# Kernel optimization log

Hardware: AMD Instinct MI355X
Metric: run time of the kernel (lower is better)

## Reference

```python
import jax, jax.numpy as jnp
import numpy as np

N, E, D, H, F = 50000, 800000, 256, 4, 32
NEG_SLOPE = 0.2

def setup_inputs() -> dict:
    key = jax.random.key(0)
    ks = jax.random.split(key, 8)
    h = jax.random.normal(ks[0], (N, D), dtype=jnp.float32)
    W = jax.random.normal(ks[1], (D, H * F), dtype=jnp.float32) * (1.0 / np.sqrt(D))
    attn_l_w = jax.random.normal(ks[2], (F, 1), dtype=jnp.float32) * (1.0 / np.sqrt(F))
    attn_l_b = jnp.zeros((1,), dtype=jnp.float32)
    attn_r_w = jax.random.normal(ks[3], (F, 1), dtype=jnp.float32) * (1.0 / np.sqrt(F))
    attn_r_b = jnp.zeros((1,), dtype=jnp.float32)
    bias = jnp.zeros((H, F), dtype=jnp.float32)
    src = jax.random.randint(ks[4], (E,), 0, N, dtype=jnp.int32)
    dst = jax.random.randint(ks[5], (E,), 0, N, dtype=jnp.int32)
    return {"h": h, "W": W, "attn_l_w": attn_l_w, "attn_l_b": attn_l_b,
            "attn_r_w": attn_r_w, "attn_r_b": attn_r_b, "bias": bias,
            "src": src, "dst": dst}

def reference(h, W, attn_l_w, attn_l_b, attn_r_w, attn_r_b, bias, src, dst):
    # node projection: [N, D] @ [D, H*F] -> [N, H, F]
    hW = (h @ W).reshape(N, H, F)
    # per-node attention halves: Dense(1) over F -> [N, H, 1]
    el = jnp.einsum('nhf,fo->nho', hW, attn_l_w) + attn_l_b
    er = jnp.einsum('nhf,fo->nho', hW, attn_r_w) + attn_r_b
    # edge logits: src contributes er, dst contributes el -> [E, H, 1]
    e = er[src] + el[dst]
    e = jnp.where(e >= 0, e, NEG_SLOPE * e)  # leaky_relu
    # segment softmax over destination groups
    emax = jax.ops.segment_max(e, dst, num_segments=N)  # [N, H, 1]
    ee = jnp.exp(e - emax[dst])
    denom = jax.ops.segment_sum(ee, dst, num_segments=N)  # [N, H, 1]
    a = ee / denom[dst]  # [E, H, 1]
    # weighted message scatter-sum: [E, H, F] -> [N, H, F]
    m = hW[src] * a
    out = jax.ops.segment_sum(m, dst, num_segments=N) + bias
    return out
```

## Files before the change

kernel.cpp:

```cpp
#include <hip/hip_runtime.h>
#include <hip/hip_bf16.h>

#define N_NODES 50000
#define E_EDGES 800000
#define D_IN    256
#define H_HEADS 4
#define HF      128
#define NEG_SLOPE 0.2f
#define SCAN_BLOCKS ((N_NODES + 255) / 256)
#define PREP_BLOCKS 128
#define ZERO_BLOCKS SCAN_BLOCKS
#define GEMM_BLOCKS ((N_NODES + 63) / 64)

#define HIST_FAT_BLOCKS 625
#define HIST_STRIDE (HIST_FAT_BLOCKS * 256)

#define FILL_BLOCKS 782
#define FILL_STRIDE (FILL_BLOCKS * 256)

typedef __attribute__((ext_vector_type(8))) short bf16x8;
typedef __attribute__((ext_vector_type(4))) float f32x4;

__device__ __forceinline__ float bf_lo(unsigned u) { return __uint_as_float(u << 16); }
__device__ __forceinline__ float bf_hi(unsigned u) { return __uint_as_float(u & 0xFFFF0000u); }

__global__ __launch_bounds__(256) void k_zero_prep(unsigned* __restrict__ cnt,
                                                   const float* __restrict__ W,
                                                   __hip_bfloat16* __restrict__ Wt) {
    const int b = blockIdx.x;
    if (b < ZERO_BLOCKS) {
        const int g = b * 256 + threadIdx.x;
        if (g < N_NODES) cnt[g] = 0u;
    } else {
        const int g = (b - ZERO_BLOCKS) * 256 + threadIdx.x;
        const int n = g >> 8;
        const int k = g & 255;
        Wt[n * D_IN + k] = __float2bfloat16(W[k * HF + n]);
    }
}

__global__ __launch_bounds__(256) void k_gemm_hist(const float* __restrict__ h,
                                                   const __hip_bfloat16* __restrict__ Wt,
                                                   const float* __restrict__ lw,
                                                   const float* __restrict__ lb,
                                                   const float* __restrict__ rw,
                                                   const float* __restrict__ rb,
                                                   __hip_bfloat16* __restrict__ hW,
                                                   float* __restrict__ el,
                                                   float* __restrict__ er,
                                                   const int* __restrict__ dst,
                                                   unsigned* __restrict__ cnt) {
    __shared__ __hip_bfloat16 As[64][72];
    __shared__ __hip_bfloat16 Bs[128][72];

    if (blockIdx.x >= GEMM_BLOCKS) {
        const int g0 = (blockIdx.x - GEMM_BLOCKS) * 256 + threadIdx.x;
        int d[5];
        #pragma unroll
        for (int i = 0; i < 5; ++i) d[i] = dst[g0 + i * HIST_STRIDE];
        #pragma unroll
        for (int i = 0; i < 5; ++i) atomicAdd(&cnt[d[i]], 1u);
        return;
    }

    const int t    = threadIdx.x;
    const int r0   = blockIdx.x * 64;
    const int wave = t >> 6;
    const int lane = t & 63;
    const int l16  = lane & 15;
    const int quad = lane >> 4;

    f32x4 acc[8] = {};

    for (int k0 = 0; k0 < D_IN; k0 += 64) {
        {
            const int row  = t >> 2;
            const int koff = (t & 3) * 16;
            const int n    = r0 + row;
            float v[16];
            if (n < N_NODES) {
                const float* p = h + (size_t)n * D_IN + k0 + koff;
                *(float4*)&v[0]  = ((const float4*)p)[0];
                *(float4*)&v[4]  = ((const float4*)p)[1];
                *(float4*)&v[8]  = ((const float4*)p)[2];
                *(float4*)&v[12] = ((const float4*)p)[3];
            } else {
                #pragma unroll
                for (int i = 0; i < 16; ++i) v[i] = 0.f;
            }
            __hip_bfloat16 b[16];
            #pragma unroll
            for (int i = 0; i < 16; ++i) b[i] = __float2bfloat16(v[i]);
            *(uint4*)&As[row][koff]     = ((uint4*)b)[0];
            *(uint4*)&As[row][koff + 8] = ((uint4*)b)[1];
        }
        {
            const int n    = t >> 1;
            const int koff = (t & 1) * 32;
            const uint4* p = (const uint4*)(Wt + n * D_IN + k0 + koff);
            uint4 b0 = p[0], b1 = p[1], b2 = p[2], b3 = p[3];
            uint4* q = (uint4*)&Bs[n][koff];
            q[0] = b0; q[1] = b1; q[2] = b2; q[3] = b3;
        }
        __syncthreads();

        #pragma unroll
        for (int ks = 0; ks < 2; ++ks) {
            const bf16x8 af = *(const bf16x8*)&As[wave * 16 + l16][ks * 32 + quad * 8];
            #pragma unroll
            for (int nt = 0; nt < 8; ++nt) {
                const bf16x8 bfg = *(const bf16x8*)&Bs[nt * 16 + l16][ks * 32 + quad * 8];
                acc[nt] = __builtin_amdgcn_mfma_f32_16x16x32_bf16(af, bfg, acc[nt], 0, 0, 0);
            }
        }
        __syncthreads();
    }

    const int mbase = r0 + wave * 16 + quad * 4;
    #pragma unroll
    for (int nt = 0; nt < 8; ++nt) {
        #pragma unroll
        for (int r = 0; r < 4; ++r) {
            const int m = mbase + r;
            if (m < N_NODES)
                hW[(size_t)m * HF + nt * 16 + l16] = __float2bfloat16(acc[nt][r]);
        }
    }

    const float lwv0 = lw[l16], lwv1 = lw[l16 + 16];
    const float rwv0 = rw[l16], rwv1 = rw[l16 + 16];
    const float lb0 = lb[0], rb0 = rb[0];
    #pragma unroll
    for (int r = 0; r < 4; ++r) {
        const int m = mbase + r;
        float el4[4], er4[4];
        #pragma unroll
        for (int hh = 0; hh < 4; ++hh) {
            float pl = acc[2 * hh][r] * lwv0 + acc[2 * hh + 1][r] * lwv1;
            float pr = acc[2 * hh][r] * rwv0 + acc[2 * hh + 1][r] * rwv1;
            #pragma unroll
            for (int o = 1; o < 16; o <<= 1) {
                pl += __shfl_xor(pl, o);
                pr += __shfl_xor(pr, o);
            }
            el4[hh] = pl + lb0;
            er4[hh] = pr + rb0;
        }
        if (l16 == 0 && m < N_NODES) {
            *(float4*)&el[m * H_HEADS] = make_float4(el4[0], el4[1], el4[2], el4[3]);
            *(float4*)&er[m * H_HEADS] = make_float4(er4[0], er4[1], er4[2], er4[3]);
        }
    }
}

__global__ __launch_bounds__(256) void k_scan(const unsigned* __restrict__ cnt,
                                              unsigned* __restrict__ off) {
    __shared__ unsigned s[256];
    const int t = threadIdx.x;
    const int b = blockIdx.x;
    const int base = b * 256;

    unsigned part = 0;
    #pragma unroll 4
    for (int i = t; i < base; i += 256) part += cnt[i];
    s[t] = part;
    __syncthreads();
    #pragma unroll
    for (int o = 128; o > 0; o >>= 1) {
        if (t < o) s[t] += s[t + o];
        __syncthreads();
    }
    const unsigned pre = s[0];
    __syncthreads();

    const int g = base + t;
    const unsigned x = (g < N_NODES) ? cnt[g] : 0u;
    s[t] = x;
    __syncthreads();
    unsigned inc = x;
    #pragma unroll
    for (int o = 1; o < 256; o <<= 1) {
        const unsigned v = (t >= o) ? s[t - o] : 0u;
        __syncthreads();
        inc += v;
        s[t] = inc;
        __syncthreads();
    }
    if (g < N_NODES) off[g] = pre + inc - x;
}

__global__ __launch_bounds__(256) void k_fill(const int* __restrict__ src,
                                              const int* __restrict__ dst,
                                              unsigned* __restrict__ off,
                                              unsigned* __restrict__ perm) {
    const int g0 = blockIdx.x * 256 + threadIdx.x;
    const int g1 = g0 + FILL_STRIDE;
    const int g2 = g1 + FILL_STRIDE;
    const int g3 = g2 + FILL_STRIDE;
    const bool ok3 = (g3 < E_EDGES);
    const int d0 = dst[g0], s0 = src[g0];
    const int d1 = dst[g1], s1 = src[g1];
    const int d2 = dst[g2], s2 = src[g2];
    const int d3 = ok3 ? dst[g3] : 0;
    const int s3 = ok3 ? src[g3] : 0;
    const unsigned p0 = atomicAdd(&off[d0], 1u);
    const unsigned p1 = atomicAdd(&off[d1], 1u);
    const unsigned p2 = atomicAdd(&off[d2], 1u);
    unsigned p3 = 0u;
    if (ok3) p3 = atomicAdd(&off[d3], 1u);
    perm[p0] = (unsigned)s0;
    perm[p1] = (unsigned)s1;
    perm[p2] = (unsigned)s2;
    if (ok3) perm[p3] = (unsigned)s3;
}

__global__ __launch_bounds__(256) void k_aggregate(const __hip_bfloat16* __restrict__ hW,
                                                   const float* __restrict__ el,
                                                   const float* __restrict__ er,
                                                   const unsigned* __restrict__ off_end,
                                                   const unsigned* __restrict__ perm,
                                                   const float* __restrict__ bias,
                                                   float* __restrict__ out) {
    const int wave = threadIdx.x >> 6;
    const int lane = threadIdx.x & 63;
    const int half = lane >> 5;
    const int l    = lane & 31;
    const int hh   = l >> 3;
    const int n    = blockIdx.x * 4 + wave;
    const unsigned beg = (n == 0) ? 0u : off_end[n - 1];
    const unsigned end = off_end[n];
    const float eld = el[(unsigned)n * H_HEADS + hh];
    const uint2* hW2 = (const uint2*)hW;

    float a0 = 0.f, a1 = 0.f, a2 = 0.f, a3 = 0.f, denom = 0.f;
    unsigned j = beg;
    for (; j + 8 <= end; j += 8) {
        const unsigned s0 = perm[j + half];
        const unsigned s1 = perm[j + 2 + half];
        const unsigned s2 = perm[j + 4 + half];
        const unsigned s3 = perm[j + 6 + half];
        const float er0 = er[s0 * H_HEADS + hh];
        const float er1 = er[s1 * H_HEADS + hh];
        const float er2 = er[s2 * H_HEADS + hh];
        const float er3 = er[s3 * H_HEADS + hh];
        const uint2 g0 = hW2[s0 * 32u + l];
        const uint2 g1 = hW2[s1 * 32u + l];
        const uint2 g2 = hW2[s2 * 32u + l];
        const uint2 g3 = hW2[s3 * 32u + l];
        float v0 = er0 + eld; v0 = (v0 >= 0.f) ? v0 : NEG_SLOPE * v0;
        float v1 = er1 + eld; v1 = (v1 >= 0.f) ? v1 : NEG_SLOPE * v1;
        float v2 = er2 + eld; v2 = (v2 >= 0.f) ? v2 : NEG_SLOPE * v2;
        float v3 = er3 + eld; v3 = (v3 >= 0.f) ? v3 : NEG_SLOPE * v3;
        const float p0 = __expf(v0);
        const float p1 = __expf(v1);
        const float p2 = __expf(v2);
        const float p3 = __expf(v3);
        denom += (p0 + p1) + (p2 + p3);
        a0 += p0 * bf_lo(g0.x) + p1 * bf_lo(g1.x) + p2 * bf_lo(g2.x) + p3 * bf_lo(g3.x);
        a1 += p0 * bf_hi(g0.x) + p1 * bf_hi(g1.x) + p2 * bf_hi(g2.x) + p3 * bf_hi(g3.x);
        a2 += p0 * bf_lo(g0.y) + p1 * bf_lo(g1.y) + p2 * bf_lo(g2.y) + p3 * bf_lo(g3.y);
        a3 += p0 * bf_hi(g0.y) + p1 * bf_hi(g1.y) + p2 * bf_hi(g2.y) + p3 * bf_hi(g3.y);
    }
    if (j + 4 <= end) {
        const unsigned s0 = perm[j + half];
        const unsigned s1 = perm[j + 2 + half];
        const float er0 = er[s0 * H_HEADS + hh];
        const float er1 = er[s1 * H_HEADS + hh];
        const uint2 g0 = hW2[s0 * 32u + l];
        const uint2 g1 = hW2[s1 * 32u + l];
        float v0 = er0 + eld; v0 = (v0 >= 0.f) ? v0 : NEG_SLOPE * v0;
        float v1 = er1 + eld; v1 = (v1 >= 0.f) ? v1 : NEG_SLOPE * v1;
        const float p0 = __expf(v0);
        const float p1 = __expf(v1);
        denom += p0 + p1;
        a0 += p0 * bf_lo(g0.x) + p1 * bf_lo(g1.x);
        a1 += p0 * bf_hi(g0.x) + p1 * bf_hi(g1.x);
        a2 += p0 * bf_lo(g0.y) + p1 * bf_lo(g1.y);
        a3 += p0 * bf_hi(g0.y) + p1 * bf_hi(g1.y);
        j += 4;
    }
    for (; j < end; j += 2) {
        const unsigned i = j + half;
        const bool ok = (i < end);
        const unsigned s = ok ? perm[i] : 0u;
        const float erv = er[s * H_HEADS + hh];
        const uint2 g = hW2[s * 32u + l];
        float v = erv + eld; v = (v >= 0.f) ? v : NEG_SLOPE * v;
        const float p = ok ? __expf(v) : 0.f;
        denom += p;
        a0 += p * bf_lo(g.x);
        a1 += p * bf_hi(g.x);
        a2 += p * bf_lo(g.y);
        a3 += p * bf_hi(g.y);
    }
    denom += __shfl_xor(denom, 32);
    a0 += __shfl_xor(a0, 32);
    a1 += __shfl_xor(a1, 32);
    a2 += __shfl_xor(a2, 32);
    a3 += __shfl_xor(a3, 32);
    if (half == 0) {
        const float inv = (end > beg) ? 1.f / denom : 0.f;
        const float4 bv = *(const float4*)&bias[l * 4];
        float4 o = make_float4(a0 * inv + bv.x, a1 * inv + bv.y,
                               a2 * inv + bv.z, a3 * inv + bv.w);
        *(float4*)&out[(unsigned)n * HF + l * 4] = o;
    }
}

extern "C" void kernel_launch(void* const* d_in, const int* in_sizes, int n_in,
                              void* d_out, int out_size, void* d_ws, size_t ws_size,
                              hipStream_t stream) {
    const float* h    = (const float*)d_in[0];
    const float* W    = (const float*)d_in[1];
    const float* lw   = (const float*)d_in[2];
    const float* lb   = (const float*)d_in[3];
    const float* rw   = (const float*)d_in[4];
    const float* rb   = (const float*)d_in[5];
    const float* bias = (const float*)d_in[6];
    const int*   src  = (const int*)d_in[7];
    const int*   dst  = (const int*)d_in[8];
    float* out = (float*)d_out;

    float*    ws   = (float*)d_ws;
    float*    el   = ws;
    float*    er   = ws + 200000;
    unsigned* cnt  = (unsigned*)(ws + 400000);
    unsigned* off  = (unsigned*)(ws + 450000);
    unsigned* perm = (unsigned*)(ws + 500000);
    __hip_bfloat16* Wt = (__hip_bfloat16*)(ws + 1300000);
    __hip_bfloat16* hW = (__hip_bfloat16*)(ws + 1320000);

    k_zero_prep<<<ZERO_BLOCKS + PREP_BLOCKS, 256, 0, stream>>>(cnt, W, Wt);
    k_gemm_hist<<<GEMM_BLOCKS + HIST_FAT_BLOCKS, 256, 0, stream>>>(
        h, Wt, lw, lb, rw, rb, hW, el, er, dst, cnt);
    k_scan<<<SCAN_BLOCKS, 256, 0, stream>>>(cnt, off);
    k_fill<<<FILL_BLOCKS, 256, 0, stream>>>(src, dst, off, perm);
    k_aggregate<<<N_NODES / 4, 256, 0, stream>>>(hW, el, er, off, perm, bias, out);
}
```

Measured before the change: 233.1 us.

## Add per-block histogram totals for scan and window CSR fill by destination range

The histogram pass now also keeps per-256-node block totals. The scan reads those totals for its block prefix, so it no longer re-reads the whole count array. The fill kernel is split into 8 destination windows: each block scans a 2048-edge slice and handles only edges whose destination falls in its window, which keeps the atomics and perm writes confined to a narrower address range for better cache locality. In exchange, the dst array is read 8 times and a second set of contended atomics is added to the histogram.

```diff
diff --git a/kernel.cpp b/kernel.cpp
--- a/kernel.cpp
+++ b/kernel.cpp
@@ -15,8 +15,10 @@
 #define HIST_FAT_BLOCKS 625
 #define HIST_STRIDE (HIST_FAT_BLOCKS * 256)
 
-#define FILL_BLOCKS 782
-#define FILL_STRIDE (FILL_BLOCKS * 256)
+#define FILL_WINDOWS 8
+#define FILL_WIN_NODES (N_NODES / FILL_WINDOWS)
+#define FILL_EDGES_PER_SLICE 2048
+#define FILL_SLICES ((E_EDGES + FILL_EDGES_PER_SLICE - 1) / FILL_EDGES_PER_SLICE)
 
 typedef __attribute__((ext_vector_type(8))) short bf16x8;
 typedef __attribute__((ext_vector_type(4))) float f32x4;
@@ -26,11 +28,13 @@
 
 __global__ __launch_bounds__(256) void k_zero_prep(unsigned* __restrict__ cnt,
                                                    const float* __restrict__ W,
-                                                   __hip_bfloat16* __restrict__ Wt) {
+                                                   __hip_bfloat16* __restrict__ Wt,
+                                                   unsigned* __restrict__ cblk) {
     const int b = blockIdx.x;
     if (b < ZERO_BLOCKS) {
         const int g = b * 256 + threadIdx.x;
         if (g < N_NODES) cnt[g] = 0u;
+        if (b == 0 && threadIdx.x < SCAN_BLOCKS) cblk[threadIdx.x] = 0u;
     } else {
         const int g = (b - ZERO_BLOCKS) * 256 + threadIdx.x;
         const int n = g >> 8;
@@ -49,7 +53,8 @@
                                                    float* __restrict__ el,
                                                    float* __restrict__ er,
                                                    const int* __restrict__ dst,
-                                                   unsigned* __restrict__ cnt) {
+                                                   unsigned* __restrict__ cnt,
+                                                   unsigned* __restrict__ cblk) {
     __shared__ __hip_bfloat16 As[64][72];
     __shared__ __hip_bfloat16 Bs[128][72];
 
@@ -60,6 +65,8 @@
         for (int i = 0; i < 5; ++i) d[i] = dst[g0 + i * HIST_STRIDE];
         #pragma unroll
         for (int i = 0; i < 5; ++i) atomicAdd(&cnt[d[i]], 1u);
+        #pragma unroll
+        for (int i = 0; i < 5; ++i) atomicAdd(&cblk[d[i] >> 8], 1u);
         return;
     }
 
@@ -154,16 +161,14 @@
 }
 
 __global__ __launch_bounds__(256) void k_scan(const unsigned* __restrict__ cnt,
-                                              unsigned* __restrict__ off) {
+                                              unsigned* __restrict__ off,
+                                              const unsigned* __restrict__ cblk) {
     __shared__ unsigned s[256];
     const int t = threadIdx.x;
     const int b = blockIdx.x;
     const int base = b * 256;
 
-    unsigned part = 0;
-    #pragma unroll 4
-    for (int i = t; i < base; i += 256) part += cnt[i];
-    s[t] = part;
+    s[t] = (t < b) ? cblk[t] : 0u;
     __syncthreads();
     #pragma unroll
     for (int o = 128; o > 0; o >>= 1) {
@@ -193,25 +198,21 @@
                                               const int* __restrict__ dst,
                                               unsigned* __restrict__ off,
                                               unsigned* __restrict__ perm) {
-    const int g0 = blockIdx.x * 256 + threadIdx.x;
-    const int g1 = g0 + FILL_STRIDE;
-    const int g2 = g1 + FILL_STRIDE;
-    const int g3 = g2 + FILL_STRIDE;
-    const bool ok3 = (g3 < E_EDGES);
-    const int d0 = dst[g0], s0 = src[g0];
-    const int d1 = dst[g1], s1 = src[g1];
-    const int d2 = dst[g2], s2 = src[g2];
-    const int d3 = ok3 ? dst[g3] : 0;
-    const int s3 = ok3 ? src[g3] : 0;
-    const unsigned p0 = atomicAdd(&off[d0], 1u);
-    const unsigned p1 = atomicAdd(&off[d1], 1u);
-    const unsigned p2 = atomicAdd(&off[d2], 1u);
-    unsigned p3 = 0u;
-    if (ok3) p3 = atomicAdd(&off[d3], 1u);
-    perm[p0] = (unsigned)s0;
-    perm[p1] = (unsigned)s1;
-    perm[p2] = (unsigned)s2;
-    if (ok3) perm[p3] = (unsigned)s3;
+    const int win   = blockIdx.x & 7;
+    const int slice = blockIdx.x >> 3;
+    const int base  = slice * FILL_EDGES_PER_SLICE + threadIdx.x;
+    const int lo    = win * FILL_WIN_NODES;
+    #pragma unroll
+    for (int i = 0; i < 8; ++i) {
+        const int g = base + i * 256;
+        if (g < E_EDGES) {
+            const int d = dst[g];
+            if ((unsigned)(d - lo) < (unsigned)FILL_WIN_NODES) {
+                const unsigned p = atomicAdd(&off[d], 1u);
+                perm[p] = (unsigned)src[g];
+            }
+        }
+    }
 }
 
 __global__ __launch_bounds__(256) void k_aggregate(const __hip_bfloat16* __restrict__ hW,
@@ -328,12 +329,13 @@
     unsigned* off  = (unsigned*)(ws + 450000);
     unsigned* perm = (unsigned*)(ws + 500000);
     __hip_bfloat16* Wt = (__hip_bfloat16*)(ws + 1300000);
+    unsigned* cblk = (unsigned*)(ws + 1316500);
     __hip_bfloat16* hW = (__hip_bfloat16*)(ws + 1320000);
 
-    k_zero_prep<<<ZERO_BLOCKS + PREP_BLOCKS, 256, 0, stream>>>(cnt, W, Wt);
+    k_zero_prep<<<ZERO_BLOCKS + PREP_BLOCKS, 256, 0, stream>>>(cnt, W, Wt, cblk);
     k_gemm_hist<<<GEMM_BLOCKS + HIST_FAT_BLOCKS, 256, 0, stream>>>(
-        h, Wt, lw, lb, rw, rb, hW, el, er, dst, cnt);
-    k_scan<<<SCAN_BLOCKS, 256, 0, stream>>>(cnt, off);
-    k_fill<<<FILL_BLOCKS, 256, 0, stream>>>(src, dst, off, perm);
+        h, Wt, lw, lb, rw, rb, hW, el, er, dst, cnt, cblk);
+    k_scan<<<SCAN_BLOCKS, 256, 0, stream>>>(cnt, off, cblk);
+    k_fill<<<FILL_SLICES * FILL_WINDOWS, 256, 0, stream>>>(src, dst, off, perm);
     k_aggregate<<<N_NODES / 4, 256, 0, stream>>>(hW, el, er, off, perm, bias, out);
 }
```

After: 647.6 us. +177.9%, slower.
